# Performance work log

Measured on AMD Instinct MI355X. Metric: run time of the kernel, lower is better.

The kernel has to match this reference:

```python
import jax, jax.numpy as jnp
import numpy as np
from jax.scipy.linalg import solve_triangular

N, S, G, D = 2048, 64, 1, 512


def setup_inputs() -> dict:
    key = jax.random.key(0)
    k1, k2, k3, k4 = jax.random.split(key, 4)
    x = jax.random.normal(k1, (N, D), jnp.float32)
    mu = jax.random.uniform(k2, (S, G, D), jnp.float32) - 0.5  # torch.rand(...) - 0.5
    omega = jax.random.normal(k3, (S, G), jnp.float32)
    # original init sets sigma_p = eye; perturb so m = A^T A has distinct eigenvalues
    sigma_p = jnp.eye(D, dtype=jnp.float32)[None, None] + 0.05 * jax.random.normal(k4, (S, G, D, D), jnp.float32)
    return {"x": x, "mu": mu, "omega": omega, "sigma_p": sigma_p}


def reference(x, mu, omega, sigma_p):
    d = x.shape[-1]
    # m = sigma_p^T @ sigma_p  (symmetric PSD), per class/component
    m = jnp.einsum('sgki,sgkj->sgij', sigma_p, sigma_p)  # (S,G,D,D)
    # torch: sigma = m + 0.01 * diag_embed(eig(m).eigenvalues.real) * eye(d)
    # m is symmetric PSD -> eigenvalues are real; eigvalsh is the batched symmetric form
    eigvals = jnp.linalg.eigvalsh(m)  # (S,G,D)
    sigma = m + 0.01 * eigvals[..., None] * jnp.eye(d, dtype=m.dtype)  # adds diag(eigvals)
    _ = jax.nn.softmax(omega, -1)  # computed in original forward but unused in output
    mu0 = mu[:, 0]        # (S,D)   only component 0 is used
    sig0 = sigma[:, 0]    # (S,D,D)
    # MultivariateNormal.log_prob via Cholesky, batched over classes and samples
    L = jnp.linalg.cholesky(sig0)               # (S,D,D)
    diff = x[None, :, :] - mu0[:, None, :]      # (S,N,D)
    z = solve_triangular(L, diff.swapaxes(-1, -2), lower=True)  # (S,D,N)
    maha = jnp.sum(z * z, axis=1)               # (S,N)
    logdet = 2.0 * jnp.sum(jnp.log(jnp.diagonal(L, axis1=-2, axis2=-1)), axis=-1)  # (S,)
    logp = -0.5 * (maha + logdet[:, None] + d * jnp.log(jnp.asarray(2.0 * np.pi, m.dtype)))
    return logp.T  # (N,S)
```

## Files before the change

### kernel.cpp

```cpp
#include <hip/hip_runtime.h>

#define D 512
#define TW 16

__device__ __forceinline__ float waveSum(float v) {
#pragma unroll
    for (int m = 32; m > 0; m >>= 1) v += __shfl_xor(v, m, 64);
    return v;
}
__device__ __forceinline__ float waveMin(float v) {
#pragma unroll
    for (int m = 32; m > 0; m >>= 1) v = fminf(v, __shfl_xor(v, m, 64));
    return v;
}
__device__ __forceinline__ float waveMax(float v) {
#pragma unroll
    for (int m = 32; m > 0; m >>= 1) v = fmaxf(v, __shfl_xor(v, m, 64));
    return v;
}

__global__ __launch_bounds__(256) void xpose_kernel(const float* __restrict__ x,
                                                    float* __restrict__ xT) {
    __shared__ float t[64][65];
    const int bx = blockIdx.x * 64;
    const int by = blockIdx.y * 64;
    const int tid = threadIdx.x;
    const int lx = tid & 63, lq = tid >> 6;
#pragma unroll
    for (int r = 0; r < 64; r += 4)
        t[r + lq][lx] = x[(size_t)(bx + r + lq) * D + by + lx];
    __syncthreads();
#pragma unroll
    for (int r = 0; r < 64; r += 4)
        xT[(size_t)(by + r + lq) * 2048 + bx + lx] = t[lx][r + lq];
}

__global__ __launch_bounds__(256) void syrk_kernel(const float* __restrict__ sp,
                                                   float* __restrict__ M) {
    const int s = blockIdx.y;
    const int I = blockIdx.x >> 3, J = blockIdx.x & 7;
    const int tx = threadIdx.x & 15, ty = threadIdx.x >> 4;
    const float* __restrict__ A = sp + (size_t)s * D * D;
    __shared__ __align__(16) float As[64 * 68];
    __shared__ __align__(16) float Bs[64 * 68];
    float acc[4][4];
#pragma unroll
    for (int r = 0; r < 4; r++)
#pragma unroll
        for (int q = 0; q < 4; q++) acc[r][q] = 0.f;

    for (int k0 = 0; k0 < D; k0 += 64) {
        for (int e = threadIdx.x; e < 4096; e += 256) {
            const int col = e & 63, kr = e >> 6;
            As[kr * 68 + col] = A[(size_t)(k0 + kr) * D + I * 64 + col];
            Bs[kr * 68 + col] = A[(size_t)(k0 + kr) * D + J * 64 + col];
        }
        __syncthreads();
#pragma unroll 4
        for (int k = 0; k < 64; k++) {
            const float4 a = *(const float4*)&As[k * 68 + 4 * ty];
            const float4 b = *(const float4*)&Bs[k * 68 + 4 * tx];
            const float av[4] = {a.x, a.y, a.z, a.w};
            const float bv[4] = {b.x, b.y, b.z, b.w};
#pragma unroll
            for (int r = 0; r < 4; r++)
#pragma unroll
                for (int q = 0; q < 4; q++) acc[r][q] += av[r] * bv[q];
        }
        __syncthreads();
    }
#pragma unroll
    for (int r = 0; r < 4; r++) {
        float4 v4;
        v4.x = acc[r][0]; v4.y = acc[r][1]; v4.z = acc[r][2]; v4.w = acc[r][3];
        const size_t off = (size_t)s * D * D + (size_t)(I * 64 + 4 * ty + r) * D + J * 64 + 4 * tx;
        *(float4*)(M + off) = v4;
    }
}

__global__ __launch_bounds__(1024) void latrd_panel(float* __restrict__ T,
                                                    float* __restrict__ Vt,
                                                    float* __restrict__ Wt,
                                                    float* __restrict__ dvec,
                                                    float* __restrict__ evec,
                                                    int ps, int jmax) {
    const int s = blockIdx.x;
    float* __restrict__ Ts = T + (size_t)s * D * D;
    float* __restrict__ Vg = Vt + (size_t)s * 32 * D;
    float* __restrict__ Wg = Wt + (size_t)s * 32 * D;
    const int tid = threadIdx.x, lane = tid & 63, wid = tid >> 6;
    const int l4 = lane & 15, quad = lane >> 4;
    extern __shared__ float sm[];
    float* __restrict__ Vs = sm;
    float* __restrict__ Ws = sm + 16896;
    float* __restrict__ vb = sm + 33792;
    float* __restrict__ pf = sm + 34304;
    float* __restrict__ c1 = sm + 34816;
    float* __restrict__ c2 = sm + 34848;
    float* __restrict__ red = sm + 34880;
    float* __restrict__ sca = sm + 34896;

    for (int i = tid; i < 34304; i += 1024) sm[i] = 0.f;
    __syncthreads();

    float rk = (tid < D) ? Ts[(size_t)ps * D + tid] : 0.f;

    for (int j = 0; j < jmax; j++) {
        const int k = ps + j, sup = k + 1;
        float val = 0.f;
        if (tid < D) pf[tid] = 0.f;
        if (tid < D && tid > k) {
            float corr = 0.f;
#pragma unroll 4
            for (int t = 0; t < j; t++)
                corr += Vs[tid * 33 + t] * Ws[k * 33 + t]
                      + Ws[tid * 33 + t] * Vs[k * 33 + t];
            val = rk - corr;
            vb[tid] = val;
            if (tid == sup) sca[3] = val;
        } else if (tid == k) {
            float dc = 0.f;
            for (int t = 0; t < j; t++) dc += Vs[k * 33 + t] * Ws[k * 33 + t];
            dvec[s * D + k] = rk - 2.f * dc;
            vb[k] = 0.f;
        }
        float xp = (tid < D && tid > sup) ? val * val : 0.f;
        xp = waveSum(xp);
        if (lane == 0) red[wid] = xp;
        __syncthreads();

        float xn2 = 0.f;
#pragma unroll
        for (int q = 0; q < TW; q++) xn2 += red[q];
        const float a0 = sca[3];
        const int skip = (xn2 <= 0.f);
        float beta = 0.f, v0 = 0.f, alpha = a0;
        if (!skip) {
            const float an = sqrtf(a0 * a0 + xn2);
            alpha = (a0 >= 0.f) ? -an : an;
            v0 = a0 - alpha;
            beta = 2.f / (v0 * v0 + xn2);
        }
        if (tid == sup) {
            evec[s * D + k] = skip ? a0 : alpha;
            if (!skip) vb[sup] = v0;
        }
        if (!skip) {
            const int t = tid >> 5, r = tid & 31;
            float a1 = 0.f, a2 = 0.f;
            for (int i = sup + 1 + r; i < D; i += 32) {
                const float v = vb[i];
                a1 += Ws[i * 33 + t] * v;
                a2 += Vs[i * 33 + t] * v;
            }
#pragma unroll
            for (int m = 16; m > 0; m >>= 1) {
                a1 += __shfl_xor(a1, m, 64);
                a2 += __shfl_xor(a2, m, 64);
            }
            if (r == 0) {
                c1[t] = a1 + Ws[sup * 33 + t] * v0;
                c2[t] = a2 + Vs[sup * 33 + t] * v0;
            }
        }
        __syncthreads();
        if (skip) {
            if (tid < D && tid >= sup) { Vg[j * D + tid] = 0.f; Wg[j * D + tid] = 0.f; }
            if (tid < D && k + 1 < D) rk = Ts[(size_t)(k + 1) * D + tid];
            __syncthreads();
            continue;
        }

        {
            const int b0 = sup >> 6, tb = 8 - b0, ntile = tb * (tb + 1) / 2;
            for (int tt = wid; tt < ntile; tt += TW) {
                int ri = 0, acc0 = 0;
                while (acc0 + ri + 1 <= tt) { acc0 += ri + 1; ri++; }
                const int cj = tt - acc0;
                const int gi0 = (b0 + ri) << 6, gj0 = (b0 + cj) << 6;
                for (int rr = quad; rr < 64; rr += 4) {
                    const float4 a = *(const float4*)&Ts[(size_t)(gi0 + rr) * D + gj0 + 4 * l4];
                    const float4 b = *(const float4*)&vb[gj0 + 4 * l4];
                    float sum = a.x * b.x + a.y * b.y + a.z * b.z + a.w * b.w;
                    sum += __shfl_xor(sum, 1, 64);
                    sum += __shfl_xor(sum, 2, 64);
                    sum += __shfl_xor(sum, 4, 64);
                    sum += __shfl_xor(sum, 8, 64);
                    if (l4 == 0) atomicAdd(&pf[gi0 + rr], sum);
                }
                if (ri != cj) {
                    const float* __restrict__ base = Ts + (size_t)gi0 * D + gj0 + lane;
                    float y0 = 0.f, y1 = 0.f, y2 = 0.f, y3 = 0.f;
#pragma unroll 4
                    for (int rr = 0; rr < 64; rr += 4) {
                        y0 += base[(size_t)(rr    ) * D] * vb[gi0 + rr];
                        y1 += base[(size_t)(rr + 1) * D] * vb[gi0 + rr + 1];
                        y2 += base[(size_t)(rr + 2) * D] * vb[gi0 + rr + 2];
                        y3 += base[(size_t)(rr + 3) * D] * vb[gi0 + rr + 3];
                    }
                    atomicAdd(&pf[gj0 + lane], (y0 + y1) + (y2 + y3));
                }
            }
        }
        __syncthreads();

        float pvp = 0.f;
        if (tid < D && tid >= sup) {
            float corr = 0.f;
#pragma unroll 8
            for (int t = 0; t < 32; t++)
                corr += Vs[tid * 33 + t] * c1[t] + Ws[tid * 33 + t] * c2[t];
            const float p = beta * (pf[tid] - corr);
            pf[tid] = p;
            pvp = p * vb[tid];
        }
        pvp = waveSum(pvp);
        if (lane == 0) red[wid] = pvp;
        __syncthreads();

        float pv = 0.f;
#pragma unroll
        for (int q = 0; q < TW; q++) pv += red[q];
        const float cc = 0.5f * beta * pv;
        if (tid < D) {
            if (tid >= sup) {
                const float v = vb[tid];
                const float w = pf[tid] - cc * v;
                Vs[tid * 33 + j] = v;
                Ws[tid * 33 + j] = w;
                Vg[j * D + tid] = v;
                Wg[j * D + tid] = w;
            }
            if (k + 1 < D) rk = Ts[(size_t)(k + 1) * D + tid];
        }
        __syncthreads();
    }
    if (ps + jmax == D - 2 && tid == 0) {
        const int k1 = D - 2, k2 = D - 1;
        float dc = 0.f, ec = 0.f, dc2 = 0.f;
        for (int t = 0; t < jmax; t++) {
            dc  += Vs[k1 * 33 + t] * Ws[k1 * 33 + t];
            ec  += Vs[k1 * 33 + t] * Ws[k2 * 33 + t]
                 + Ws[k1 * 33 + t] * Vs[k2 * 33 + t];
            dc2 += Vs[k2 * 33 + t] * Ws[k2 * 33 + t];
        }
        dvec[s * D + k1] = Ts[(size_t)k1 * D + k1] - 2.f * dc;
        evec[s * D + k1] = Ts[(size_t)k1 * D + k2] - ec;
        dvec[s * D + k2] = Ts[(size_t)k2 * D + k2] - 2.f * dc2;
        evec[s * D + k2] = 0.f;
    }
}

__global__ __launch_bounds__(256) void latrd_update(float* __restrict__ T,
                                                    const float* __restrict__ Vt,
                                                    const float* __restrict__ Wt,
                                                    int r0) {
    const int s = blockIdx.z;
    const int i0 = r0 + 64 * blockIdx.y;
    const int j0 = r0 + 64 * blockIdx.x;
    float* __restrict__ Ts = T + (size_t)s * D * D;
    const float* __restrict__ Vg = Vt + (size_t)s * 32 * D;
    const float* __restrict__ Wg = Wt + (size_t)s * 32 * D;
    __shared__ __align__(16) float Vi[32 * 68], Wi[32 * 68], Vj[32 * 68], Wj[32 * 68];
    const int tid = threadIdx.x, tx = tid & 15, ty = tid >> 4;
    const float4 z4 = {0.f, 0.f, 0.f, 0.f};
    for (int e = tid; e < 512; e += 256) {
        const int t = e >> 4, c4 = (e & 15) * 4;
        const int gi = i0 + c4, gj = j0 + c4;
        *(float4*)&Vi[t * 68 + c4] = (gi < D) ? *(const float4*)&Vg[t * D + gi] : z4;
        *(float4*)&Wi[t * 68 + c4] = (gi < D) ? *(const float4*)&Wg[t * D + gi] : z4;
        *(float4*)&Vj[t * 68 + c4] = (gj < D) ? *(const float4*)&Vg[t * D + gj] : z4;
        *(float4*)&Wj[t * 68 + c4] = (gj < D) ? *(const float4*)&Wg[t * D + gj] : z4;
    }
    __syncthreads();
    float acc[4][4] = {{0.f}};
#pragma unroll 4
    for (int t = 0; t < 32; t++) {
        const float4 va = *(const float4*)&Vi[t * 68 + 4 * ty];
        const float4 wa = *(const float4*)&Wi[t * 68 + 4 * ty];
        const float4 vc = *(const float4*)&Vj[t * 68 + 4 * tx];
        const float4 wc = *(const float4*)&Wj[t * 68 + 4 * tx];
        const float av[4] = {va.x, va.y, va.z, va.w};
        const float aw[4] = {wa.x, wa.y, wa.z, wa.w};
        const float bv[4] = {vc.x, vc.y, vc.z, vc.w};
        const float bw[4] = {wc.x, wc.y, wc.z, wc.w};
#pragma unroll
        for (int r = 0; r < 4; r++)
#pragma unroll
            for (int q = 0; q < 4; q++) acc[r][q] += av[r] * bw[q] + aw[r] * bv[q];
    }
    const int gj = j0 + 4 * tx;
    if (gj >= D) return;
#pragma unroll
    for (int r = 0; r < 4; r++) {
        const int gi = i0 + 4 * ty + r;
        if (gi >= D) continue;
        float4 c = *(float4*)&Ts[(size_t)gi * D + gj];
        c.x -= acc[r][0]; c.y -= acc[r][1]; c.z -= acc[r][2]; c.w -= acc[r][3];
        *(float4*)&Ts[(size_t)gi * D + gj] = c;
    }
}

__global__ __launch_bounds__(128) void bisect_kernel(const float* __restrict__ dvec,
                                                     const float* __restrict__ evec,
                                                     float* __restrict__ lam) {
    const int s = blockIdx.y, seg = blockIdx.x;
    const int tid = threadIdx.x;
    __shared__ float d[D], e2c[D], ea[D];
    __shared__ float rlo[2], rhi[2];
    for (int i = tid; i < D; i += 128) {
        d[i] = dvec[s * D + i];
        const float ev = evec[s * D + i];
        ea[i] = fabsf(ev);
        e2c[i] = fmaxf(ev * ev, 1e-34f);
    }
    __syncthreads();
    float lo = 1e30f, hi = -1e30f;
    for (int i = tid; i < D; i += 128) {
        const float rad = ea[i] + ((i > 0) ? ea[i - 1] : 0.f);
        lo = fminf(lo, d[i] - rad);
        hi = fmaxf(hi, d[i] + rad);
    }
    lo = waveMin(lo); hi = waveMax(hi);
    if ((tid & 63) == 0) { rlo[tid >> 6] = lo; rhi[tid >> 6] = hi; }
    __syncthreads();
    lo = fminf(rlo[0], rlo[1]); hi = fmaxf(rhi[0], rhi[1]);
    lo -= 1e-3f * fmaxf(fabsf(lo), 1.f);
    hi += 1e-3f * fmaxf(fabsf(hi), 1.f);
    float a = lo, b = hi;
    const int j1 = seg * 128 + tid + 1;
    for (int it = 0; it < 26; it++) {
        const float mid = 0.5f * (a + b);
        int cnt = 0;
        float q = d[0] - mid;
        cnt += (q < 0.f);
        for (int i = 1; i < D; i++) {
            q = d[i] - mid - e2c[i - 1] * __builtin_amdgcn_rcpf(q);
            cnt += (q < 0.f);
        }
        if (cnt >= j1) b = mid; else a = mid;
    }
    lam[s * D + seg * 128 + tid] = 0.5f * (a + b);
}

__global__ __launch_bounds__(256) void chol_panel(float* __restrict__ M,
                                                  const float* __restrict__ lam,
                                                  float* __restrict__ logdet,
                                                  float* __restrict__ Lp,
                                                  int j0, int first) {
    const int s = blockIdx.x;
    float* __restrict__ Ms = M + (size_t)s * D * D;
    float* __restrict__ Lps = Lp + (size_t)s * 32 * D;
    const int tid = threadIdx.x, lane = tid & 63, wid = tid >> 6;
    extern __shared__ float smc[];
    float* __restrict__ P = smc;
    const int Wd = D - j0;
    for (int e = tid; e < 32 * D; e += 256) {
        const int t = e >> 9, i = e & 511;
        if (i >= j0) {
            const int il = i - j0;
            float v = Ms[(size_t)(j0 + t) * D + i];
            if (il == t) v += 0.01f * lam[s * D + j0 + t];
            P[t * 520 + il] = v;
        }
    }
    __syncthreads();
    float lacc = 0.f;
    for (int jl = 0; jl < 32; jl++) {
        const float pd = P[jl * 520 + jl];
        const float inv = 1.f / sqrtf(pd);
        if (tid == 0) { lacc += 0.5f * logf(pd); P[jl * 520 + jl] = sqrtf(pd); }
        for (int il = jl + 1 + tid; il < Wd; il += 256) P[jl * 520 + il] *= inv;
        __syncthreads();
        for (int kk = jl + 1 + wid; kk < 32; kk += 4) {
            const float f = P[jl * 520 + kk];
            for (int il = kk + lane; il < Wd; il += 64) P[kk * 520 + il] -= f * P[jl * 520 + il];
        }
        __syncthreads();
    }
    if (tid == 0) logdet[s] = (first ? 0.f : logdet[s]) + 2.f * lacc;
    for (int e = tid; e < 32 * D; e += 256) {
        const int t = e >> 9, i = e & 511;
        const int il = i - j0;
        if (il >= t) Ms[(size_t)(j0 + t) * D + i] = P[t * 520 + il];
        if (i >= j0 + 32) Lps[(size_t)t * D + i] = P[t * 520 + il];
    }
}

__global__ __launch_bounds__(256) void chol_update(float* __restrict__ M,
                                                   const float* __restrict__ Lp,
                                                   int r0) {
    if (blockIdx.x < blockIdx.y) return;
    const int s = blockIdx.z;
    const int i0 = r0 + 64 * blockIdx.y;
    const int j0 = r0 + 64 * blockIdx.x;
    float* __restrict__ Ms = M + (size_t)s * D * D;
    const float* __restrict__ Lps = Lp + (size_t)s * 32 * D;
    __shared__ __align__(16) float Li[32 * 68], Lj[32 * 68];
    const int tid = threadIdx.x, tx = tid & 15, ty = tid >> 4;
    const float4 z4 = {0.f, 0.f, 0.f, 0.f};
    for (int e = tid; e < 512; e += 256) {
        const int t = e >> 4, c4 = (e & 15) * 4;
        const int gi = i0 + c4, gj = j0 + c4;
        *(float4*)&Li[t * 68 + c4] = (gi < D) ? *(const float4*)&Lps[(size_t)t * D + gi] : z4;
        *(float4*)&Lj[t * 68 + c4] = (gj < D) ? *(const float4*)&Lps[(size_t)t * D + gj] : z4;
    }
    __syncthreads();
    float acc[4][4] = {{0.f}};
#pragma unroll 4
    for (int t = 0; t < 32; t++) {
        const float4 a = *(const float4*)&Li[t * 68 + 4 * ty];
        const float4 b = *(const float4*)&Lj[t * 68 + 4 * tx];
        const float av[4] = {a.x, a.y, a.z, a.w};
        const float bv[4] = {b.x, b.y, b.z, b.w};
#pragma unroll
        for (int r = 0; r < 4; r++)
#pragma unroll
            for (int q = 0; q < 4; q++) acc[r][q] += av[r] * bv[q];
    }
    const int gj = j0 + 4 * tx;
    if (gj >= D) return;
#pragma unroll
    for (int r = 0; r < 4; r++) {
        const int gi = i0 + 4 * ty + r;
        if (gi >= D) continue;
        float4 c = *(float4*)&Ms[(size_t)gi * D + gj];
        c.x -= acc[r][0]; c.y -= acc[r][1]; c.z -= acc[r][2]; c.w -= acc[r][3];
        *(float4*)&Ms[(size_t)gi * D + gj] = c;
    }
}

__global__ __launch_bounds__(64) void invdiag_kernel(const float* __restrict__ M,
                                                     float* __restrict__ invDT) {
    const int b = blockIdx.x, s = b >> 3, I = b & 7;
    const int c = threadIdx.x;
    __shared__ float Lsh[64 * 65];
    __shared__ float xsh[64 * 65];
    const float* __restrict__ Ms = M + (size_t)s * D * D;
    for (int e = c; e < 4096; e += 64) {
        const int i = e & 63, k = e >> 6;
        Lsh[i * 65 + k] = Ms[(size_t)(I * 64 + k) * D + I * 64 + i];
    }
    for (int i = 0; i < 64; i++) xsh[c * 65 + i] = (i == c) ? 1.f : 0.f;
    __syncthreads();
    for (int i = 0; i < 64; i++) {
        float t = xsh[c * 65 + i];
        for (int k = 0; k < i; k++) t -= Lsh[i * 65 + k] * xsh[c * 65 + k];
        xsh[c * 65 + i] = t / Lsh[i * 65 + i];
    }
    float* __restrict__ outp = invDT + (size_t)b * 4096 + c * 64;
    for (int i = 0; i < 64; i++) outp[i] = xsh[c * 65 + i];
}

__global__ __launch_bounds__(256) void triinv_step(float* __restrict__ M,
                                                   const float* __restrict__ invDT,
                                                   int I) {
    const int J = blockIdx.x, s = blockIdx.y;
    float* __restrict__ Ms = M + (size_t)s * D * D;
    __shared__ __align__(16) float Ls[64 * 68];
    __shared__ __align__(16) float Bs[64 * 68];
    __shared__ __align__(16) float Ss[64 * 68];
    const int tid = threadIdx.x, tx = tid & 15, ty = tid >> 4;
    float acc[4][4] = {{0.f}};
    for (int K = J; K < I; K++) {
        __syncthreads();
        for (int e = tid; e < 4096; e += 256) {
            const int k = e >> 6, r = e & 63;
            Ls[k * 68 + r] = Ms[(size_t)(K * 64 + k) * D + I * 64 + r];
        }
        if (K == J) {
            const float* __restrict__ dJ = invDT + ((size_t)s * 8 + J) * 4096;
            for (int e = tid; e < 4096; e += 256) {
                const int c = e >> 6, k = e & 63;
                Bs[k * 68 + c] = dJ[c * 64 + k];
            }
        } else {
            for (int e = tid; e < 4096; e += 256) {
                const int k = e >> 6, c = e & 63;
                Bs[k * 68 + c] = Ms[(size_t)(K * 64 + k) * D + J * 64 + c];
            }
        }
        __syncthreads();
#pragma unroll 4
        for (int k = 0; k < 64; k++) {
            const float4 a = *(const float4*)&Ls[k * 68 + 4 * ty];
            const float4 b = *(const float4*)&Bs[k * 68 + 4 * tx];
            const float av[4] = {a.x, a.y, a.z, a.w};
            const float bv[4] = {b.x, b.y, b.z, b.w};
#pragma unroll
            for (int r = 0; r < 4; r++)
#pragma unroll
                for (int q = 0; q < 4; q++) acc[r][q] += av[r] * bv[q];
        }
    }
    __syncthreads();
#pragma unroll
    for (int r = 0; r < 4; r++) {
        float4 v4;
        v4.x = acc[r][0]; v4.y = acc[r][1]; v4.z = acc[r][2]; v4.w = acc[r][3];
        *(float4*)&Ss[(4 * ty + r) * 68 + 4 * tx] = v4;
    }
    {
        const float* __restrict__ dI = invDT + ((size_t)s * 8 + I) * 4096;
        for (int e = tid; e < 4096; e += 256) {
            const int k = e >> 6, r = e & 63;
            Ls[k * 68 + r] = dI[k * 64 + r];
        }
    }
    __syncthreads();
    float o[4][4] = {{0.f}};
#pragma unroll 4
    for (int k = 0; k < 64; k++) {
        const float4 a = *(const float4*)&Ls[k * 68 + 4 * ty];
        const float4 b = *(const float4*)&Ss[k * 68 + 4 * tx];
        const float av[4] = {a.x, a.y, a.z, a.w};
        const float bv[4] = {b.x, b.y, b.z, b.w};
#pragma unroll
        for (int r = 0; r < 4; r++)
#pragma unroll
            for (int q = 0; q < 4; q++) o[r][q] += av[r] * bv[q];
    }
#pragma unroll
    for (int r = 0; r < 4; r++) {
        float4 v4;
        v4.x = -o[r][0]; v4.y = -o[r][1]; v4.z = -o[r][2]; v4.w = -o[r][3];
        *(float4*)&Ms[(size_t)(I * 64 + 4 * ty + r) * D + J * 64 + 4 * tx] = v4;
    }
}

__global__ __launch_bounds__(256) void gemm_maha(const float* __restrict__ M,
                                                 const float* __restrict__ invDT,
                                                 const float* __restrict__ xT,
                                                 const float* __restrict__ mu,
                                                 const float* __restrict__ logdet,
                                                 float* __restrict__ out) {
    const int s = blockIdx.y;
    const int n0 = blockIdx.x * 64;
    const int tid = threadIdx.x, tx = tid & 15, ty = tid >> 4;
    const float* __restrict__ Ms = M + (size_t)s * D * D;
    const float* __restrict__ mus = mu + s * D;
    __shared__ __align__(16) float As[32 * 136];
    __shared__ __align__(16) float Bs[32 * 68];
    __shared__ float red[16 * 68];
    float cs[4] = {0.f, 0.f, 0.f, 0.f};

    for (int ci = 0; ci < 4; ci++) {
        const int i0 = ci * 128;
        float acc[8][4];
#pragma unroll
        for (int r = 0; r < 8; r++)
#pragma unroll
            for (int q = 0; q < 4; q++) acc[r][q] = 0.f;
        const int nkc = (ci + 1) * 4;
        for (int kc = 0; kc < nkc; kc++) {
            const int k0 = kc * 32, kb = k0 >> 6;
            __syncthreads();
            for (int e = tid; e < 4096; e += 256) {
                const int il = e >> 5, kk = e & 31;
                const int ib = (i0 + il) >> 6;
                As[kk * 136 + il] = (kb < ib) ? Ms[(size_t)(i0 + il) * D + k0 + kk] : 0.f;
            }
            if (kb >= 2 * ci) {
                const float* __restrict__ dB = invDT + ((size_t)s * 8 + kb) * 4096
                                             + (size_t)(k0 & 63) * 64;
                const int ilb = (kb - 2 * ci) * 64;
                for (int e = tid; e < 2048; e += 256) {
                    const int ii = e & 63, kk = e >> 6;
                    As[kk * 136 + ilb + ii] = dB[kk * 64 + ii];
                }
            }
            for (int e = tid; e < 2048; e += 256) {
                const int nn = e & 63, kk = e >> 6;
                Bs[kk * 68 + nn] = xT[(size_t)(k0 + kk) * 2048 + n0 + nn] - mus[k0 + kk];
            }
            __syncthreads();
#pragma unroll 8
            for (int kk = 0; kk < 32; kk++) {
                const float4 a0 = *(const float4*)&As[kk * 136 + 8 * ty];
                const float4 a1 = *(const float4*)&As[kk * 136 + 8 * ty + 4];
                const float4 b  = *(const float4*)&Bs[kk * 68 + 4 * tx];
                const float av[8] = {a0.x, a0.y, a0.z, a0.w, a1.x, a1.y, a1.z, a1.w};
                const float bv[4] = {b.x, b.y, b.z, b.w};
#pragma unroll
                for (int r = 0; r < 8; r++)
#pragma unroll
                    for (int q = 0; q < 4; q++) acc[r][q] += av[r] * bv[q];
            }
        }
#pragma unroll
        for (int r = 0; r < 8; r++)
#pragma unroll
            for (int q = 0; q < 4; q++) cs[q] += acc[r][q] * acc[r][q];
    }
    __syncthreads();
#pragma unroll
    for (int q = 0; q < 4; q++) red[ty * 68 + 4 * tx + q] = cs[q];
    __syncthreads();
    if (tid < 64) {
        float mah = 0.f;
#pragma unroll
        for (int t = 0; t < 16; t++) mah += red[t * 68 + tid];
        out[(size_t)(n0 + tid) * 64 + s] = -0.5f * (mah + logdet[s] + 940.993058f);
    }
}

extern "C" void kernel_launch(void* const* d_in, const int* in_sizes, int n_in,
                              void* d_out, int out_size, void* d_ws, size_t ws_size,
                              hipStream_t stream) {
    const float* x  = (const float*)d_in[0];
    const float* mu = (const float*)d_in[1];
    const float* sp = (const float*)d_in[3];
    float* out = (float*)d_out;

    float* wsf  = (float*)d_ws;
    float* MT   = wsf;
    float* dvec = wsf + (size_t)16777216;
    float* evec = dvec + 32768;
    float* lamv = evec + 32768;
    float* logd = lamv + 32768;
    float* Vt   = logd + 64;
    float* Wt   = Vt + (size_t)1048576;
    float* xT   = Wt + (size_t)1048576;
    float* Lp   = Vt;
    float* invDT = Vt;

    xpose_kernel<<<dim3(32, 8), dim3(256), 0, stream>>>(x, xT);
    syrk_kernel<<<dim3(64, 64), dim3(256), 0, stream>>>(sp, MT);

    const size_t plds = (size_t)34900 * sizeof(float);
    for (int p = 0; p < 16; p++) {
        const int ps = 32 * p;
        const int jmax = (p == 15) ? 30 : 32;
        latrd_panel<<<dim3(64), dim3(1024), plds, stream>>>(MT, Vt, Wt, dvec, evec, ps, jmax);
        if (p < 15) {
            const int r0 = ps + 32;
            const int nt = (D - r0 + 63) / 64;
            latrd_update<<<dim3(nt, nt, 64), dim3(256), 0, stream>>>(MT, Vt, Wt, r0);
        }
    }

    bisect_kernel<<<dim3(4, 64), dim3(128), 0, stream>>>(dvec, evec, lamv);

    syrk_kernel<<<dim3(64, 64), dim3(256), 0, stream>>>(sp, MT);
    const size_t clds = (size_t)(32 * 520 + 4) * sizeof(float);
    for (int p = 0; p < 16; p++) {
        const int j0 = 32 * p;
        chol_panel<<<dim3(64), dim3(256), clds, stream>>>(MT, lamv, logd, Lp, j0, p == 0 ? 1 : 0);
        if (p < 15) {
            const int r0 = j0 + 32;
            const int nt = (D - r0 + 63) / 64;
            chol_update<<<dim3(nt, nt, 64), dim3(256), 0, stream>>>(MT, Lp, r0);
        }
    }

    invdiag_kernel<<<dim3(512), dim3(64), 0, stream>>>(MT, invDT);
    for (int I = 1; I < 8; I++)
        triinv_step<<<dim3(I, 64), dim3(256), 0, stream>>>(MT, invDT, I);

    gemm_maha<<<dim3(32, 64), dim3(256), 0, stream>>>(MT, invDT, xT, mu, logd, out);
}
```

Measured before the change: 12.09 ms.

## Restructure LATRD panel matvec to use full rows and fold corrections algebraically

The panel's symmetric matrix-vector product over triangular tiles with atomicAdd scatter is replaced by a row-wise pass over the full trailing rows, which avoids shared-memory atomics. The V/W corrections are fused into that pass, and the rank-2 scalar is computed as beta squared times (vAv minus two c1·c2), which removes one reduction and one sync. V/W shared rows are padded to 34 so they can be read as float2, and the fixed-length correction loop depends on the zero-initialised padding. The Mahalanobis kernel's A tile is moved to a row-major layout filled with float4 loads, at the cost of scalar strided reads in the inner loop.

Result: faster. 9.739 ms (-19.4%).

```diff
diff --git a/kernel.cpp b/kernel.cpp
--- a/kernel.cpp
+++ b/kernel.cpp
@@ -92,15 +92,15 @@
     const int l4 = lane & 15, quad = lane >> 4;
     extern __shared__ float sm[];
     float* __restrict__ Vs = sm;
-    float* __restrict__ Ws = sm + 16896;
-    float* __restrict__ vb = sm + 33792;
-    float* __restrict__ pf = sm + 34304;
-    float* __restrict__ c1 = sm + 34816;
-    float* __restrict__ c2 = sm + 34848;
-    float* __restrict__ red = sm + 34880;
-    float* __restrict__ sca = sm + 34896;
-
-    for (int i = tid; i < 34304; i += 1024) sm[i] = 0.f;
+    float* __restrict__ Ws = sm + 17408;
+    float* __restrict__ vb = sm + 34816;
+    float* __restrict__ pf = sm + 35328;
+    float* __restrict__ c1 = sm + 35840;
+    float* __restrict__ c2 = sm + 35872;
+    float* __restrict__ red = sm + 35904;
+    float* __restrict__ sca = sm + 35920;
+
+    for (int i = tid; i < 35328; i += 1024) sm[i] = 0.f;
     __syncthreads();
 
     float rk = (tid < D) ? Ts[(size_t)ps * D + tid] : 0.f;
@@ -108,19 +108,28 @@
     for (int j = 0; j < jmax; j++) {
         const int k = ps + j, sup = k + 1;
         float val = 0.f;
-        if (tid < D) pf[tid] = 0.f;
         if (tid < D && tid > k) {
+            const float* __restrict__ vrow = Vs + tid * 34;
+            const float* __restrict__ wrow = Ws + tid * 34;
+            const float* __restrict__ vk = Vs + k * 34;
+            const float* __restrict__ wk = Ws + k * 34;
             float corr = 0.f;
-#pragma unroll 4
-            for (int t = 0; t < j; t++)
-                corr += Vs[tid * 33 + t] * Ws[k * 33 + t]
-                      + Ws[tid * 33 + t] * Vs[k * 33 + t];
+#pragma unroll
+            for (int t = 0; t < 32; t += 2) {
+                const float2 a  = *(const float2*)&vrow[t];
+                const float2 bw = *(const float2*)&wk[t];
+                const float2 aw = *(const float2*)&wrow[t];
+                const float2 bv = *(const float2*)&vk[t];
+                corr += a.x * bw.x + a.y * bw.y + aw.x * bv.x + aw.y * bv.y;
+            }
             val = rk - corr;
             vb[tid] = val;
             if (tid == sup) sca[3] = val;
         } else if (tid == k) {
+            const float* __restrict__ vk = Vs + k * 34;
+            const float* __restrict__ wk = Ws + k * 34;
             float dc = 0.f;
-            for (int t = 0; t < j; t++) dc += Vs[k * 33 + t] * Ws[k * 33 + t];
+            for (int t = 0; t < 32; t++) dc += vk[t] * wk[t];
             dvec[s * D + k] = rk - 2.f * dc;
             vb[k] = 0.f;
         }
@@ -150,8 +159,8 @@
             float a1 = 0.f, a2 = 0.f;
             for (int i = sup + 1 + r; i < D; i += 32) {
                 const float v = vb[i];
-                a1 += Ws[i * 33 + t] * v;
-                a2 += Vs[i * 33 + t] * v;
+                a1 += Ws[i * 34 + t] * v;
+                a2 += Vs[i * 34 + t] * v;
             }
 #pragma unroll
             for (int m = 16; m > 0; m >>= 1) {
@@ -159,8 +168,8 @@
                 a2 += __shfl_xor(a2, m, 64);
             }
             if (r == 0) {
-                c1[t] = a1 + Ws[sup * 33 + t] * v0;
-                c2[t] = a2 + Vs[sup * 33 + t] * v0;
+                c1[t] = a1 + Ws[sup * 34 + t] * v0;
+                c2[t] = a2 + Vs[sup * 34 + t] * v0;
             }
         }
         __syncthreads();
@@ -170,64 +179,48 @@
             __syncthreads();
             continue;
         }
-
-        {
-            const int b0 = sup >> 6, tb = 8 - b0, ntile = tb * (tb + 1) / 2;
-            for (int tt = wid; tt < ntile; tt += TW) {
-                int ri = 0, acc0 = 0;
-                while (acc0 + ri + 1 <= tt) { acc0 += ri + 1; ri++; }
-                const int cj = tt - acc0;
-                const int gi0 = (b0 + ri) << 6, gj0 = (b0 + cj) << 6;
-                for (int rr = quad; rr < 64; rr += 4) {
-                    const float4 a = *(const float4*)&Ts[(size_t)(gi0 + rr) * D + gj0 + 4 * l4];
-                    const float4 b = *(const float4*)&vb[gj0 + 4 * l4];
-                    float sum = a.x * b.x + a.y * b.y + a.z * b.z + a.w * b.w;
-                    sum += __shfl_xor(sum, 1, 64);
-                    sum += __shfl_xor(sum, 2, 64);
-                    sum += __shfl_xor(sum, 4, 64);
-                    sum += __shfl_xor(sum, 8, 64);
-                    if (l4 == 0) atomicAdd(&pf[gi0 + rr], sum);
-                }
-                if (ri != cj) {
-                    const float* __restrict__ base = Ts + (size_t)gi0 * D + gj0 + lane;
-                    float y0 = 0.f, y1 = 0.f, y2 = 0.f, y3 = 0.f;
-#pragma unroll 4
-                    for (int rr = 0; rr < 64; rr += 4) {
-                        y0 += base[(size_t)(rr    ) * D] * vb[gi0 + rr];
-                        y1 += base[(size_t)(rr + 1) * D] * vb[gi0 + rr + 1];
-                        y2 += base[(size_t)(rr + 2) * D] * vb[gi0 + rr + 2];
-                        y3 += base[(size_t)(rr + 3) * D] * vb[gi0 + rr + 3];
-                    }
-                    atomicAdd(&pf[gj0 + lane], (y0 + y1) + (y2 + y3));
-                }
-            }
-        }
-        __syncthreads();
-
-        float pvp = 0.f;
-        if (tid < D && tid >= sup) {
-            float corr = 0.f;
-#pragma unroll 8
-            for (int t = 0; t < 32; t++)
-                corr += Vs[tid * 33 + t] * c1[t] + Ws[tid * 33 + t] * c2[t];
-            const float p = beta * (pf[tid] - corr);
-            pf[tid] = p;
-            pvp = p * vb[tid];
-        }
-        pvp = waveSum(pvp);
-        if (lane == 0) red[wid] = pvp;
-        __syncthreads();
-
-        float pv = 0.f;
-#pragma unroll
-        for (int q = 0; q < TW; q++) pv += red[q];
-        const float cc = 0.5f * beta * pv;
+        float c12 = 0.f;
+#pragma unroll
+        for (int t = 0; t < 32; t += 4) {
+            const float4 ca = *(const float4*)&c1[t];
+            const float4 cb = *(const float4*)&c2[t];
+            c12 += ca.x * cb.x + ca.y * cb.y + ca.z * cb.z + ca.w * cb.w;
+        }
+
+        const int w0 = sup & ~63;
+        float vAvp = 0.f;
+        for (int i = sup + (wid * 4 + quad); i < D; i += 64) {
+            const float* __restrict__ row = Ts + (size_t)i * D;
+            float4 a4 = {0.f, 0.f, 0.f, 0.f};
+            for (int c = w0 + 4 * l4; c < D; c += 64) {
+                const float4 a = *(const float4*)&row[c];
+                const float4 b = *(const float4*)&vb[c];
+                a4.x += a.x * b.x; a4.y += a.y * b.y;
+                a4.z += a.z * b.z; a4.w += a.w * b.w;
+            }
+            const float raw = (a4.x + a4.y) + (a4.z + a4.w);
+            vAvp += vb[i] * raw;
+            float t1 = raw
+                - (Vs[i * 34 + l4] * c1[l4] + Vs[i * 34 + l4 + 16] * c1[l4 + 16]
+                 + Ws[i * 34 + l4] * c2[l4] + Ws[i * 34 + l4 + 16] * c2[l4 + 16]);
+#pragma unroll
+            for (int m = 1; m < 16; m <<= 1) t1 += __shfl_xor(t1, m, 64);
+            if (l4 == 0) pf[i] = t1;
+        }
+        vAvp = waveSum(vAvp);
+        if (lane == 0) red[wid] = vAvp;
+        __syncthreads();
+
+        float vAv = 0.f;
+#pragma unroll
+        for (int q = 0; q < TW; q++) vAv += red[q];
+        const float cc = 0.5f * beta * beta * (vAv - 2.f * c12);
         if (tid < D) {
             if (tid >= sup) {
                 const float v = vb[tid];
-                const float w = pf[tid] - cc * v;
-                Vs[tid * 33 + j] = v;
-                Ws[tid * 33 + j] = w;
+                const float w = beta * pf[tid] - cc * v;
+                Vs[tid * 34 + j] = v;
+                Ws[tid * 34 + j] = w;
                 Vg[j * D + tid] = v;
                 Wg[j * D + tid] = w;
             }
@@ -239,10 +232,10 @@
         const int k1 = D - 2, k2 = D - 1;
         float dc = 0.f, ec = 0.f, dc2 = 0.f;
         for (int t = 0; t < jmax; t++) {
-            dc  += Vs[k1 * 33 + t] * Ws[k1 * 33 + t];
-            ec  += Vs[k1 * 33 + t] * Ws[k2 * 33 + t]
-                 + Ws[k1 * 33 + t] * Vs[k2 * 33 + t];
-            dc2 += Vs[k2 * 33 + t] * Ws[k2 * 33 + t];
+            dc  += Vs[k1 * 34 + t] * Ws[k1 * 34 + t];
+            ec  += Vs[k1 * 34 + t] * Ws[k2 * 34 + t]
+                 + Ws[k1 * 34 + t] * Vs[k2 * 34 + t];
+            dc2 += Vs[k2 * 34 + t] * Ws[k2 * 34 + t];
         }
         dvec[s * D + k1] = Ts[(size_t)k1 * D + k1] - 2.f * dc;
         evec[s * D + k1] = Ts[(size_t)k1 * D + k2] - ec;
@@ -539,7 +532,7 @@
     const int tid = threadIdx.x, tx = tid & 15, ty = tid >> 4;
     const float* __restrict__ Ms = M + (size_t)s * D * D;
     const float* __restrict__ mus = mu + s * D;
-    __shared__ __align__(16) float As[32 * 136];
+    __shared__ __align__(16) float As[128 * 36];
     __shared__ __align__(16) float Bs[32 * 68];
     __shared__ float red[16 * 68];
     float cs[4] = {0.f, 0.f, 0.f, 0.f};
@@ -555,10 +548,18 @@
         for (int kc = 0; kc < nkc; kc++) {
             const int k0 = kc * 32, kb = k0 >> 6;
             __syncthreads();
-            for (int e = tid; e < 4096; e += 256) {
-                const int il = e >> 5, kk = e & 31;
-                const int ib = (i0 + il) >> 6;
-                As[kk * 136 + il] = (kb < ib) ? Ms[(size_t)(i0 + il) * D + k0 + kk] : 0.f;
+            {
+                const int g = tid & 7, il0 = tid >> 3;
+#pragma unroll
+                for (int p = 0; p < 4; p++) {
+                    const int il = il0 + 32 * p;
+                    const int ib = (i0 + il) >> 6;
+                    if (ib != kb) {
+                        float4 v = {0.f, 0.f, 0.f, 0.f};
+                        if (kb < ib) v = *(const float4*)&Ms[(size_t)(i0 + il) * D + k0 + 4 * g];
+                        *(float4*)&As[il * 36 + 4 * g] = v;
+                    }
+                }
             }
             if (kb >= 2 * ci) {
                 const float* __restrict__ dB = invDT + ((size_t)s * 8 + kb) * 4096
@@ -566,7 +567,7 @@
                 const int ilb = (kb - 2 * ci) * 64;
                 for (int e = tid; e < 2048; e += 256) {
                     const int ii = e & 63, kk = e >> 6;
-                    As[kk * 136 + ilb + ii] = dB[kk * 64 + ii];
+                    As[(ilb + ii) * 36 + kk] = dB[kk * 64 + ii];
                 }
             }
             for (int e = tid; e < 2048; e += 256) {
@@ -574,13 +575,13 @@
                 Bs[kk * 68 + nn] = xT[(size_t)(k0 + kk) * 2048 + n0 + nn] - mus[k0 + kk];
             }
             __syncthreads();
-#pragma unroll 8
+#pragma unroll 4
             for (int kk = 0; kk < 32; kk++) {
-                const float4 a0 = *(const float4*)&As[kk * 136 + 8 * ty];
-                const float4 a1 = *(const float4*)&As[kk * 136 + 8 * ty + 4];
-                const float4 b  = *(const float4*)&Bs[kk * 68 + 4 * tx];
-                const float av[8] = {a0.x, a0.y, a0.z, a0.w, a1.x, a1.y, a1.z, a1.w};
+                const float4 b = *(const float4*)&Bs[kk * 68 + 4 * tx];
                 const float bv[4] = {b.x, b.y, b.z, b.w};
+                float av[8];
+#pragma unroll
+                for (int r = 0; r < 8; r++) av[r] = As[(8 * ty + r) * 36 + kk];
 #pragma unroll
                 for (int r = 0; r < 8; r++)
 #pragma unroll
@@ -627,7 +628,7 @@
     xpose_kernel<<<dim3(32, 8), dim3(256), 0, stream>>>(x, xT);
     syrk_kernel<<<dim3(64, 64), dim3(256), 0, stream>>>(sp, MT);
 
-    const size_t plds = (size_t)34900 * sizeof(float);
+    const size_t plds = (size_t)35924 * sizeof(float);
     for (int p = 0; p < 16; p++) {
         const int ps = 32 * p;
         const int jmax = (p == 15) ? 30 : 32;
```
